# Kernel optimization log

Hardware: AMD Instinct MI355X
Metric: run time of the kernel (lower is better)

The kernel has to match this reference:

```python
import jax, jax.numpy as jnp
import numpy as np
from jax import lax

H, W = 2048, 2048  # output_size


def setup_inputs() -> dict:
    key = jax.random.key(0)
    # normalized [ymin, xmin, ymax, xmax] in [0,1]; invalid (min>=max) boxes are
    # naturally skipped by the empty-mask logic, same as the torch `continue`.
    boxes = jax.random.uniform(key, (1024, 4), dtype=jnp.float32)
    return {"boxes": boxes}


def reference(boxes):
    ys = jnp.arange(H, dtype=jnp.int32)  # [H]
    xs = jnp.arange(W, dtype=jnp.int32)  # [W]

    def paint(smap, box):
        # pixel coords: truncate toward zero like torch .long(), then clamp
        y1 = jnp.maximum(0, (box[0] * H).astype(jnp.int32))
        x1 = jnp.maximum(0, (box[1] * W).astype(jnp.int32))
        y2 = jnp.minimum(H, (box[2] * H).astype(jnp.int32))
        x2 = jnp.minimum(W, (box[3] * W).astype(jnp.int32))
        cover = ((ys >= y1) & (ys < y2))[:, None] & ((xs >= x1) & (xs < x2))[None, :]  # [H,W]
        # channel values: [1.0, ymin, xmin, ymax, xmax] (normalized box coords)
        vals = jnp.concatenate([jnp.ones((1,), boxes.dtype), box])  # [5]
        # later boxes overwrite earlier ones inside their rectangle (paint order)
        new_map = jnp.where(cover[None, :, :], vals[:, None, None], smap)
        return new_map, None

    smap0 = jnp.zeros((5, H, W), dtype=boxes.dtype)
    smap, _ = lax.scan(paint, smap0, boxes)
    return smap[None]  # (1, 5, H, W)
```

## Files before the change

kernel.cpp:

```cpp
#include <hip/hip_runtime.h>

#define HH 2048
#define WW 2048
#define NB 1024
#define NT 512
#define BANDH 8
#define NSTRIP 16
#define SW 128
#define CAP 64


__global__ __launch_bounds__(NT, 2) void paint_kernel(const float4* __restrict__ boxes,
                                                      float* __restrict__ out) {
    __shared__ uint2 coordS[NB];
    __shared__ unsigned long long fmS[NSTRIP][2][8];
    __shared__ unsigned long long imS[NSTRIP][2][8];
    __shared__ uint2 clistS[NSTRIP][CAP];
    __shared__ short cidxS[NSTRIP][CAP];
    __shared__ int lastFullS[NSTRIP];
    __shared__ int cntS[NSTRIP];

    const int tid  = threadIdx.x;
    const int lane = tid & 63;
    const int wid  = tid >> 6;
    const int band  = ((blockIdx.x & 7) << 5) | (blockIdx.x >> 3);
    const int tileY = band * BANDH;

    unsigned im16[2], fm16[2];
    #pragma unroll
    for (int c = 0; c < 2; ++c) {
        float4 bx = boxes[c * NT + tid];
        int y1 = max(0, (int)(bx.x * (float)HH));
        int x1 = max(0, (int)(bx.y * (float)WW));
        int y2 = min(HH, (int)(bx.z * (float)HH));
        int x2 = min(WW, (int)(bx.w * (float)WW));
        coordS[c * NT + tid] = make_uint2(((unsigned)y1 << 16) | (unsigned)x1,
                                          ((unsigned)y2 << 16) | (unsigned)x2);
        bool valid = (y1 < y2) && (x1 < x2);
        bool yint  = valid && (y1 < tileY + BANDH) && (y2 > tileY);
        bool yfull = valid && (y1 <= tileY) && (y2 >= tileY + BANDH);
        int ilo = x1 >> 7, ihi = min(NSTRIP, (x2 + SW - 1) >> 7);
        unsigned imask = 0;
        if (yint && ihi > ilo) imask = (unsigned)(((1u << (ihi - ilo)) - 1u) << ilo);
        int clo = (x1 + SW - 1) >> 7, chi = x2 >> 7;
        unsigned cmask = 0;
        if (yfull && chi > clo) cmask = (unsigned)(((1u << (chi - clo)) - 1u) << clo);
        im16[c] = imask; fm16[c] = cmask;
    }
    #pragma unroll
    for (int c = 0; c < 2; ++c)
        #pragma unroll
        for (int s = 0; s < NSTRIP; ++s) {
            unsigned long long bi = __ballot((im16[c] >> s) & 1);
            unsigned long long bf = __ballot((fm16[c] >> s) & 1);
            if (lane == 0) { imS[s][c][wid] = bi; fmS[s][c][wid] = bf; }
        }
    __syncthreads();

    if (tid < NSTRIP) {
        const int s = tid;
        int lf = -1;
        for (int c = 1; c >= 0 && lf < 0; --c)
            for (int w = 7; w >= 0 && lf < 0; --w) {
                unsigned long long m = fmS[s][c][w];
                if (m) lf = c * 512 + w * 64 + 63 - __clzll(m);
            }
        lastFullS[s] = lf;
        int j = 0;
        for (int c = 0; c < 2; ++c)
            for (int w = 0; w < 8; ++w) {
                unsigned long long m = imS[s][c][w];
                int base = c * 512 + w * 64;
                int d = lf - base;
                if (d >= 63) m = 0;
                else if (d >= 0) m &= (~0ull) << (d + 1);
                while (m) {
                    int b = base + __builtin_ctzll(m);
                    m &= m - 1;
                    if (j < CAP) { clistS[s][j] = coordS[b]; cidxS[s][j] = (short)b; }
                    ++j;
                }
            }
        cntS[s] = (j <= CAP) ? j : -1;
    }
    __syncthreads();

    const int py = tileY + wid;
    const int lx = lane << 2;
    int fnd[8][4];
    bool uni[8];
    #pragma unroll
    for (int xi = 0; xi < 8; ++xi) {
        const int s   = xi * 2 + (lane >> 5);
        const int px0 = xi * 256 + lx;
        const int lf  = lastFullS[s];
        int f0 = lf, f1 = lf, f2 = lf, f3 = lf;
        const int c = cntS[s];
        if (c >= 0) {
            for (int j = 0; j < c; ++j) {
                uint2 pc = clistS[s][j];
                int bidx = cidxS[s][j];
                int by1 = (int)(pc.x >> 16), bx1 = (int)(pc.x & 0xffffu);
                int by2 = (int)(pc.y >> 16), bx2 = (int)(pc.y & 0xffffu);
                if (py >= by1 && py < by2) {
                    if (px0     >= bx1 && px0     < bx2) f0 = bidx;
                    if (px0 + 1 >= bx1 && px0 + 1 < bx2) f1 = bidx;
                    if (px0 + 2 >= bx1 && px0 + 2 < bx2) f2 = bidx;
                    if (px0 + 3 >= bx1 && px0 + 3 < bx2) f3 = bidx;
                }
            }
        } else {
            for (int b = lf + 1; b < NB; ++b) {
                uint2 pc = coordS[b];
                int by1 = (int)(pc.x >> 16), bx1 = (int)(pc.x & 0xffffu);
                int by2 = (int)(pc.y >> 16), bx2 = (int)(pc.y & 0xffffu);
                if (py >= by1 && py < by2) {
                    if (px0     >= bx1 && px0     < bx2) f0 = b;
                    if (px0 + 1 >= bx1 && px0 + 1 < bx2) f1 = b;
                    if (px0 + 2 >= bx1 && px0 + 2 < bx2) f2 = b;
                    if (px0 + 3 >= bx1 && px0 + 3 < bx2) f3 = b;
                }
            }
        }
        fnd[xi][0] = f0; fnd[xi][1] = f1; fnd[xi][2] = f2; fnd[xi][3] = f3;
        uni[xi] = (f0 == f1) && (f1 == f2) && (f2 == f3);
    }

    const float* bfp = (const float*)boxes;
    #pragma unroll
    for (int ch = 0; ch < 5; ++ch) {
        float* op = out + (size_t)ch * ((size_t)HH * WW) + (size_t)py * WW;
        #pragma unroll
        for (int xi = 0; xi < 8; ++xi) {
            float4 v;
            if (uni[xi]) {
                int f = fnd[xi][0];
                float val;
                if (ch == 0) val = (f >= 0) ? 1.f : 0.f;
                else         val = (f >= 0) ? bfp[f * 4 + (ch - 1)] : 0.f;
                v = make_float4(val, val, val, val);
            } else {
                #pragma unroll
                for (int k = 0; k < 4; ++k) {
                    int f = fnd[xi][k];
                    float val;
                    if (ch == 0) val = (f >= 0) ? 1.f : 0.f;
                    else         val = (f >= 0) ? bfp[f * 4 + (ch - 1)] : 0.f;
                    ((float*)&v)[k] = val;
                }
            }
            *(float4*)(op + xi * 256 + lx) = v;
        }
    }
}

extern "C" void kernel_launch(void* const* d_in, const int* in_sizes, int n_in,
                              void* d_out, int out_size, void* d_ws, size_t ws_size,
                              hipStream_t stream) {
    const float4* boxes = (const float4*)d_in[0];
    float* out = (float*)d_out;
    dim3 grid(HH / BANDH);
    dim3 block(NT);
    paint_kernel<<<grid, block, 0, stream>>>(boxes, out);
}
```

Before: 102.1 us.

## Split painting into mask, tile-list and per-channel paint kernels via workspace

Replaces the single fused kernel with three launches. The first builds per-row-band and per-column-strip intersection and full-cover bitmasks. The second combines them into per-tile (32x128) candidate lists and last-full-box indices. The third paints one channel per block over 4-row bands. This spreads the box scan and list construction across many blocks instead of repeating it per band, and gives far more, smaller blocks for the store-bound output. In exchange it adds two extra launches and workspace round trips, and it recomputes the per-pixel box search once per channel instead of once for all five.

Result: slower. 123.1 us (+20.5%).

```diff
diff --git a/kernel.cpp b/kernel.cpp
--- a/kernel.cpp
+++ b/kernel.cpp
@@ -3,106 +3,148 @@
 #define HH 2048
 #define WW 2048
 #define NB 1024
-#define NT 512
-#define BANDH 8
-#define NSTRIP 16
-#define SW 128
-#define CAP 64
+#define TW 128
+#define TH 32
+#define NTX 16
+#define NTY 64
+#define NTILE 2048
+#define CAP 32
 
+typedef float f32x4 __attribute__((ext_vector_type(4)));
+typedef unsigned long long u64;
 
-__global__ __launch_bounds__(NT, 2) void paint_kernel(const float4* __restrict__ boxes,
-                                                      float* __restrict__ out) {
-    __shared__ uint2 coordS[NB];
-    __shared__ unsigned long long fmS[NSTRIP][2][8];
-    __shared__ unsigned long long imS[NSTRIP][2][8];
-    __shared__ uint2 clistS[NSTRIP][CAP];
-    __shared__ short cidxS[NSTRIP][CAP];
-    __shared__ int lastFullS[NSTRIP];
-    __shared__ int cntS[NSTRIP];
+#define OFF_COORD  0
+#define OFF_YINT   8192
+#define OFF_YFULL  16384
+#define OFF_XINT   24576
+#define OFF_XFULL  26624
+#define OFF_LF     28672
+#define OFF_CNT    36864
+#define OFF_ENT    45056
+#define OFF_IDX    569344
 
-    const int tid  = threadIdx.x;
-    const int lane = tid & 63;
-    const int wid  = tid >> 6;
-    const int band  = ((blockIdx.x & 7) << 5) | (blockIdx.x >> 3);
-    const int tileY = band * BANDH;
-
-    unsigned im16[2], fm16[2];
+__global__ __launch_bounds__(256) void k1_masks(const float4* __restrict__ boxes,
+                                                char* __restrict__ ws) {
+    uint2* coordsW = (uint2*)(ws + OFF_COORD);
+    const int tid = threadIdx.x, lane = tid & 63, wid = tid >> 6;
+    const int bid = blockIdx.x;
+    const bool isY = bid < NTY;
+    const int lo0 = isY ? (bid * TH) : ((bid - NTY) * TW);
+    const int ext = isY ? TH : TW;
+    u64* intW  = isY ? ((u64*)(ws + OFF_YINT)  + bid * 16)
+                     : ((u64*)(ws + OFF_XINT)  + (bid - NTY) * 16);
+    u64* fullW = isY ? ((u64*)(ws + OFF_YFULL) + bid * 16)
+                     : ((u64*)(ws + OFF_XFULL) + (bid - NTY) * 16);
     #pragma unroll
-    for (int c = 0; c < 2; ++c) {
-        float4 bx = boxes[c * NT + tid];
+    for (int c = 0; c < 4; ++c) {
+        float4 bx = boxes[c * 256 + tid];
         int y1 = max(0, (int)(bx.x * (float)HH));
         int x1 = max(0, (int)(bx.y * (float)WW));
         int y2 = min(HH, (int)(bx.z * (float)HH));
         int x2 = min(WW, (int)(bx.w * (float)WW));
-        coordS[c * NT + tid] = make_uint2(((unsigned)y1 << 16) | (unsigned)x1,
-                                          ((unsigned)y2 << 16) | (unsigned)x2);
+        if (bid == 0)
+            coordsW[c * 256 + tid] = make_uint2(((unsigned)y1 << 16) | (unsigned)x1,
+                                                ((unsigned)y2 << 16) | (unsigned)x2);
         bool valid = (y1 < y2) && (x1 < x2);
-        bool yint  = valid && (y1 < tileY + BANDH) && (y2 > tileY);
-        bool yfull = valid && (y1 <= tileY) && (y2 >= tileY + BANDH);
-        int ilo = x1 >> 7, ihi = min(NSTRIP, (x2 + SW - 1) >> 7);
-        unsigned imask = 0;
-        if (yint && ihi > ilo) imask = (unsigned)(((1u << (ihi - ilo)) - 1u) << ilo);
-        int clo = (x1 + SW - 1) >> 7, chi = x2 >> 7;
-        unsigned cmask = 0;
-        if (yfull && chi > clo) cmask = (unsigned)(((1u << (chi - clo)) - 1u) << clo);
-        im16[c] = imask; fm16[c] = cmask;
+        int a1 = isY ? y1 : x1, a2 = isY ? y2 : x2;
+        bool bi = valid && (a1 < lo0 + ext) && (a2 > lo0);
+        bool bf = valid && (a1 <= lo0) && (a2 >= lo0 + ext);
+        u64 mi = __ballot(bi), mf = __ballot(bf);
+        if (lane == 0) { intW[c * 4 + wid] = mi; fullW[c * 4 + wid] = mf; }
     }
+}
+
+__global__ __launch_bounds__(256) void k2_tiles(char* __restrict__ ws) {
+    const uint2* coordsW = (const uint2*)(ws + OFF_COORD);
+    const u64* yintW  = (const u64*)(ws + OFF_YINT);
+    const u64* yfullW = (const u64*)(ws + OFF_YFULL);
+    const u64* xintW  = (const u64*)(ws + OFF_XINT);
+    const u64* xfullW = (const u64*)(ws + OFF_XFULL);
+    int* lfW  = (int*)(ws + OFF_LF);
+    int* cntW = (int*)(ws + OFF_CNT);
+    uint2* entW = (uint2*)(ws + OFF_ENT);
+    short* idxW = (short*)(ws + OFF_IDX);
+
+    const int tix = blockIdx.x * 256 + threadIdx.x;
+    const int ty = tix >> 4, tx = tix & 15;
+
+    u64 iw[16];
     #pragma unroll
-    for (int c = 0; c < 2; ++c)
-        #pragma unroll
-        for (int s = 0; s < NSTRIP; ++s) {
-            unsigned long long bi = __ballot((im16[c] >> s) & 1);
-            unsigned long long bf = __ballot((fm16[c] >> s) & 1);
-            if (lane == 0) { imS[s][c][wid] = bi; fmS[s][c][wid] = bf; }
+    for (int c = 0; c < 16; ++c) iw[c] = yintW[ty * 16 + c] & xintW[tx * 16 + c];
+    int lf = -1;
+    #pragma unroll
+    for (int c = 15; c >= 0; --c)
+        if (lf < 0) {
+            u64 fw = yfullW[ty * 16 + c] & xfullW[tx * 16 + c];
+            if (fw) lf = c * 64 + 63 - __clzll(fw);
         }
-    __syncthreads();
+    int j = 0;
+    for (int c = 0; c < 16; ++c) {
+        u64 m = iw[c];
+        int d = lf - c * 64;
+        if (d >= 63) m = 0;
+        else if (d >= 0) m &= (~0ull) << (d + 1);
+        while (m) {
+            int b = c * 64 + __builtin_ctzll(m);
+            m &= m - 1;
+            if (j < CAP) { entW[tix * CAP + j] = coordsW[b]; idxW[tix * CAP + j] = (short)b; }
+            ++j;
+        }
+    }
+    lfW[tix] = lf;
+    cntW[tix] = (j <= CAP) ? j : -1;
+}
 
-    if (tid < NSTRIP) {
-        const int s = tid;
-        int lf = -1;
-        for (int c = 1; c >= 0 && lf < 0; --c)
-            for (int w = 7; w >= 0 && lf < 0; --w) {
-                unsigned long long m = fmS[s][c][w];
-                if (m) lf = c * 512 + w * 64 + 63 - __clzll(m);
-            }
-        lastFullS[s] = lf;
-        int j = 0;
-        for (int c = 0; c < 2; ++c)
-            for (int w = 0; w < 8; ++w) {
-                unsigned long long m = imS[s][c][w];
-                int base = c * 512 + w * 64;
-                int d = lf - base;
-                if (d >= 63) m = 0;
-                else if (d >= 0) m &= (~0ull) << (d + 1);
-                while (m) {
-                    int b = base + __builtin_ctzll(m);
-                    m &= m - 1;
-                    if (j < CAP) { clistS[s][j] = coordS[b]; cidxS[s][j] = (short)b; }
-                    ++j;
-                }
-            }
-        cntS[s] = (j <= CAP) ? j : -1;
+__global__ __launch_bounds__(256, 8) void k3_paint(const float4* __restrict__ boxes,
+                                                   const char* __restrict__ ws,
+                                                   float* __restrict__ out) {
+    __shared__ int lfL[NTX], cntL[NTX];
+    __shared__ uint2 entL[NTX][CAP];
+    __shared__ short idxL[NTX][CAP];
+
+    const int tid = threadIdx.x;
+    const int job  = (blockIdx.x & 7) * 320 + (blockIdx.x >> 3);
+    const int ch   = job >> 9;
+    const int band = job & 511;
+    const int y0   = band * 4;
+    const int ty   = y0 >> 5;
+
+    const int* lfW  = (const int*)(ws + OFF_LF);
+    const int* cntW = (const int*)(ws + OFF_CNT);
+    const uint2* entW = (const uint2*)(ws + OFF_ENT);
+    const short* idxW = (const short*)(ws + OFF_IDX);
+    const uint2* coordsW = (const uint2*)(ws + OFF_COORD);
+
+    if (tid < NTX) {
+        int tix = ty * NTX + tid;
+        int lf = lfW[tix], c = cntW[tix];
+        lfL[tid] = lf; cntL[tid] = c;
+        int n = (c < 0) ? 0 : c;
+        for (int j = 0; j < n; ++j) {
+            entL[tid][j] = entW[tix * CAP + j];
+            idxL[tid][j] = idxW[tix * CAP + j];
+        }
     }
     __syncthreads();
 
-    const int py = tileY + wid;
-    const int lx = lane << 2;
-    int fnd[8][4];
-    bool uni[8];
+    const int r = tid >> 6, lane = tid & 63;
+    const int y = y0 + r;
+    const float* bfp = (const float*)boxes;
+    float* op = out + (size_t)ch * ((size_t)HH * WW) + (size_t)y * WW;
+
     #pragma unroll
-    for (int xi = 0; xi < 8; ++xi) {
-        const int s   = xi * 2 + (lane >> 5);
-        const int px0 = xi * 256 + lx;
-        const int lf  = lastFullS[s];
+    for (int k = 0; k < 8; ++k) {
+        const int px0 = lane * 4 + k * 256;
+        const int s = px0 >> 7;
+        const int lf = lfL[s], cnt = cntL[s];
         int f0 = lf, f1 = lf, f2 = lf, f3 = lf;
-        const int c = cntS[s];
-        if (c >= 0) {
-            for (int j = 0; j < c; ++j) {
-                uint2 pc = clistS[s][j];
-                int bidx = cidxS[s][j];
+        if (cnt >= 0) {
+            for (int j = 0; j < cnt; ++j) {
+                uint2 pc = entL[s][j];
+                int bidx = idxL[s][j];
                 int by1 = (int)(pc.x >> 16), bx1 = (int)(pc.x & 0xffffu);
                 int by2 = (int)(pc.y >> 16), bx2 = (int)(pc.y & 0xffffu);
-                if (py >= by1 && py < by2) {
+                if (y >= by1 && y < by2) {
                     if (px0     >= bx1 && px0     < bx2) f0 = bidx;
                     if (px0 + 1 >= bx1 && px0 + 1 < bx2) f1 = bidx;
                     if (px0 + 2 >= bx1 && px0 + 2 < bx2) f2 = bidx;
@@ -111,10 +153,10 @@
             }
         } else {
             for (int b = lf + 1; b < NB; ++b) {
-                uint2 pc = coordS[b];
+                uint2 pc = coordsW[b];
                 int by1 = (int)(pc.x >> 16), bx1 = (int)(pc.x & 0xffffu);
                 int by2 = (int)(pc.y >> 16), bx2 = (int)(pc.y & 0xffffu);
-                if (py >= by1 && py < by2) {
+                if (y >= by1 && y < by2) {
                     if (px0     >= bx1 && px0     < bx2) f0 = b;
                     if (px0 + 1 >= bx1 && px0 + 1 < bx2) f1 = b;
                     if (px0 + 2 >= bx1 && px0 + 2 < bx2) f2 = b;
@@ -122,35 +164,17 @@
                 }
             }
         }
-        fnd[xi][0] = f0; fnd[xi][1] = f1; fnd[xi][2] = f2; fnd[xi][3] = f3;
-        uni[xi] = (f0 == f1) && (f1 == f2) && (f2 == f3);
-    }
-
-    const float* bfp = (const float*)boxes;
-    #pragma unroll
-    for (int ch = 0; ch < 5; ++ch) {
-        float* op = out + (size_t)ch * ((size_t)HH * WW) + (size_t)py * WW;
-        #pragma unroll
-        for (int xi = 0; xi < 8; ++xi) {
-            float4 v;
-            if (uni[xi]) {
-                int f = fnd[xi][0];
-                float val;
-                if (ch == 0) val = (f >= 0) ? 1.f : 0.f;
-                else         val = (f >= 0) ? bfp[f * 4 + (ch - 1)] : 0.f;
-                v = make_float4(val, val, val, val);
-            } else {
-                #pragma unroll
-                for (int k = 0; k < 4; ++k) {
-                    int f = fnd[xi][k];
-                    float val;
-                    if (ch == 0) val = (f >= 0) ? 1.f : 0.f;
-                    else         val = (f >= 0) ? bfp[f * 4 + (ch - 1)] : 0.f;
-                    ((float*)&v)[k] = val;
-                }
-            }
-            *(float4*)(op + xi * 256 + lx) = v;
+        f32x4 v;
+        if (f0 == f1 && f1 == f2 && f2 == f3) {
+            float val = (f0 < 0) ? 0.f : ((ch == 0) ? 1.f : bfp[f0 * 4 + (ch - 1)]);
+            v = (f32x4){val, val, val, val};
+        } else {
+            v.x = (f0 < 0) ? 0.f : ((ch == 0) ? 1.f : bfp[f0 * 4 + (ch - 1)]);
+            v.y = (f1 < 0) ? 0.f : ((ch == 0) ? 1.f : bfp[f1 * 4 + (ch - 1)]);
+            v.z = (f2 < 0) ? 0.f : ((ch == 0) ? 1.f : bfp[f2 * 4 + (ch - 1)]);
+            v.w = (f3 < 0) ? 0.f : ((ch == 0) ? 1.f : bfp[f3 * 4 + (ch - 1)]);
         }
+        *(f32x4*)(op + px0) = v;
     }
 }
 
@@ -159,7 +183,8 @@
                               hipStream_t stream) {
     const float4* boxes = (const float4*)d_in[0];
     float* out = (float*)d_out;
-    dim3 grid(HH / BANDH);
-    dim3 block(NT);
-    paint_kernel<<<grid, block, 0, stream>>>(boxes, out);
+    char* ws = (char*)d_ws;
+    k1_masks<<<dim3(NTY + NTX), dim3(256), 0, stream>>>(boxes, ws);
+    k2_tiles<<<dim3(NTILE / 256), dim3(256), 0, stream>>>(ws);
+    k3_paint<<<dim3(5 * 512), dim3(256), 0, stream>>>(boxes, ws, out);
 }
```
